# Performance work log

Hardware: AMD Instinct MI355X
Metric: run time of the kernel (lower is better)

## Reference

```python
import jax, jax.numpy as jnp
import numpy as np

N_NODES = 50000
N_EDGES = 800000
D = 128


def _graph_conv(x, W, b, src, dst, n_nodes):
    """DGL GraphConv with norm='both': D_in^{-1/2} A D_out^{-1/2} X W + b."""
    ones = jnp.ones((src.shape[0],), dtype=x.dtype)
    out_deg = jax.ops.segment_sum(ones, src, num_segments=n_nodes)
    in_deg = jax.ops.segment_sum(ones, dst, num_segments=n_nodes)
    out_norm = jax.lax.rsqrt(jnp.maximum(out_deg, 1.0))  # [N]
    in_norm = jax.lax.rsqrt(jnp.maximum(in_deg, 1.0))    # [N]
    # scale src features, transform (in_feats == out_feats so order is free), aggregate
    h = (x * out_norm[:, None]) @ W                       # [N, D]
    msgs = h[src]                                         # [E, D] gather
    agg = jax.ops.segment_sum(msgs, dst, num_segments=n_nodes)  # [N, D] scatter-add
    return agg * in_norm[:, None] + b


def setup_inputs() -> dict:
    key = jax.random.key(0)
    ks = jax.random.split(key, 8)
    x = jax.random.normal(ks[0], (N_NODES, D), dtype=jnp.float32)
    src = jax.random.randint(ks[1], (N_EDGES,), 0, N_NODES, dtype=jnp.int64)
    dst = jax.random.randint(ks[2], (N_EDGES,), 0, N_NODES, dtype=jnp.int64)
    scale = 1.0 / np.sqrt(D)
    W1 = jax.random.normal(ks[3], (D, D), dtype=jnp.float32) * scale
    W2 = jax.random.normal(ks[4], (D, D), dtype=jnp.float32) * scale
    W3 = jax.random.normal(ks[5], (D, D), dtype=jnp.float32) * scale
    b1 = jnp.zeros((D,), dtype=jnp.float32)
    b2 = jnp.zeros((D,), dtype=jnp.float32)
    b3 = jnp.zeros((D,), dtype=jnp.float32)
    return {"x": x, "src": src, "dst": dst,
            "W1": W1, "b1": b1, "W2": W2, "b2": b2, "W3": W3, "b3": b3}


def reference(x, src, dst, W1, b1, W2, b2, W3, b3):
    h = _graph_conv(x, W1, b1, src, dst, N_NODES)
    h = jax.nn.relu(h)
    h = _graph_conv(h, W2, b2, src, dst, N_NODES)
    h = jax.nn.relu(h)
    h = _graph_conv(h, W3, b3, src, dst, N_NODES)
    return h
```

## Files before the change

### kernel.cpp

```cpp
#include <hip/hip_runtime.h>
#include <hip/hip_fp16.h>

#define D 128
#define HB 128
#define HT 1024
#define WMAX 12800

struct alignas(16) H8 { __half2 h[4]; };
typedef _Float16 v8h __attribute__((ext_vector_type(8)));
typedef float v4f __attribute__((ext_vector_type(4)));

__global__ __launch_bounds__(HT) void hist_kernel(const int* __restrict__ src,
                                                  const int* __restrict__ dst,
                                                  unsigned* __restrict__ partial_out,
                                                  unsigned* __restrict__ partial_in,
                                                  unsigned char* __restrict__ lrank,
                                                  const float* __restrict__ W1,
                                                  const float* __restrict__ W2,
                                                  const float* __restrict__ W3,
                                                  _Float16* __restrict__ wt,
                                                  int nE, int W, int epb) {
    const int t = threadIdx.x;
    if ((int)blockIdx.x >= 2 * HB) {
        const int l = blockIdx.x - 2 * HB;
        const float* Wsrc = (l == 0) ? W1 : ((l == 1) ? W2 : W3);
        _Float16* o = wt + (size_t)l * D * D;
        for (int i = t; i < D * D; i += HT) {
            const int k = i >> 7, n = i & 127;
            o[n * D + k] = (_Float16)Wsrc[i];
        }
        return;
    }
    __shared__ unsigned lcnt[WMAX];
    const bool is_dst = (blockIdx.x < HB);
    const int b = is_dst ? blockIdx.x : (blockIdx.x - HB);
    for (int i = t; i < W; i += HT) lcnt[i] = 0;
    __syncthreads();
    const int e0 = b * epb;
    const int e1 = min(nE, e0 + epb);
    if (is_dst) {
        for (int e = e0 + t; e < e1; e += HT) {
            const int d = dst[e];
            const unsigned sh = (unsigned)(d & 3) * 8u;
            const unsigned old = atomicAdd(&lcnt[d >> 2], 1u << sh);
            lrank[e] = (unsigned char)((old >> sh) & 0xffu);
        }
    } else {
        for (int e = e0 + t; e < e1; e += HT) {
            const int s = src[e];
            atomicAdd(&lcnt[s >> 2], 1u << ((unsigned)(s & 3) * 8u));
        }
    }
    __syncthreads();
    unsigned* g = (is_dst ? partial_in : partial_out) + (size_t)b * W;
    for (int i = t; i < W; i += HT) g[i] = lcnt[i];
}

__global__ __launch_bounds__(256) void reduce_hist_kernel(const unsigned* __restrict__ partial_out,
                                                          const unsigned* __restrict__ partial_in,
                                                          unsigned* __restrict__ offs_in,
                                                          int* __restrict__ cnt_out,
                                                          int* __restrict__ cnt_in,
                                                          int W, int n, int nbW) {
    const bool is_dst = ((int)blockIdx.x < nbW);
    const int w = (is_dst ? blockIdx.x : (blockIdx.x - nbW)) * 256 + threadIdx.x;
    if (w >= W) return;
    unsigned run = 0;
    if (is_dst) {
#pragma unroll 16
        for (int b = 0; b < HB; ++b) {
            const unsigned c = partial_in[(size_t)b * W + w];
            offs_in[(size_t)b * W + w] = run;
            run += c;
        }
    } else {
#pragma unroll 16
        for (int b = 0; b < HB; ++b) run += partial_out[(size_t)b * W + w];
    }
    int* cnt = is_dst ? cnt_in : cnt_out;
    const int n0 = w * 4;
    const int4 c4 = make_int4((int)(run & 0xffu), (int)((run >> 8) & 0xffu),
                              (int)((run >> 16) & 0xffu), (int)((run >> 24) & 0xffu));
    if (n0 + 3 < n) {
        *(int4*)&cnt[n0] = c4;
    } else {
        const int* cp = &c4.x;
        for (int i = 0; i < 4 && n0 + i < n; ++i) cnt[n0 + i] = cp[i];
    }
}

__global__ __launch_bounds__(1024) void scan_block_kernel(const int* __restrict__ deg,
                                                          int* __restrict__ rp,
                                                          int* __restrict__ bsum, int n) {
    __shared__ int wsum[16];
    const int t = threadIdx.x;
    const int lane = t & 63;
    const int wid = t >> 6;
    const int i = blockIdx.x * 1024 + t;
    const int v = (i < n) ? deg[i] : 0;
    int s = v;
#pragma unroll
    for (int off = 1; off < 64; off <<= 1) {
        int u = __shfl_up(s, off, 64);
        if (lane >= off) s += u;
    }
    if (lane == 63) wsum[wid] = s;
    __syncthreads();
    if (wid == 0) {
        int ws = (lane < 16) ? wsum[lane] : 0;
#pragma unroll
        for (int off = 1; off < 16; off <<= 1) {
            int u = __shfl_up(ws, off, 64);
            if (lane >= off) ws += u;
        }
        if (lane < 16) wsum[lane] = ws;
    }
    __syncthreads();
    const int excl = s - v + ((wid > 0) ? wsum[wid - 1] : 0);
    if (i < n) rp[i] = excl;
    if (t == 0) bsum[blockIdx.x] = wsum[15];
}

__global__ __launch_bounds__(1024) void finalize_kernel(int* __restrict__ rp,
                                                        const int* __restrict__ bsum,
                                                        const int* __restrict__ cnt_out,
                                                        const int* __restrict__ cnt_in,
                                                        float* __restrict__ onorm,
                                                        float* __restrict__ inorm,
                                                        int n, int nb, int nE) {
    __shared__ int prefix_s;
    const int t = threadIdx.x;
    if (t < 64) {
        int v = (t < nb && t < (int)blockIdx.x) ? bsum[t] : 0;
#pragma unroll
        for (int off = 1; off < 64; off <<= 1) v += __shfl_xor(v, off, 64);
        if (t == 0) prefix_s = v;
    }
    __syncthreads();
    const int i = blockIdx.x * 1024 + t;
    if (i < n) {
        rp[i] += prefix_s;
        onorm[i] = rsqrtf(fmaxf((float)cnt_out[i], 1.0f));
        inorm[i] = rsqrtf(fmaxf((float)cnt_in[i], 1.0f));
    }
    if (blockIdx.x == 0 && t == 0) rp[n] = nE;
}

__global__ __launch_bounds__(1024) void gemm1_fill_kernel(
    const float* __restrict__ x, const _Float16* __restrict__ wt,
    const float* __restrict__ onorm, __half* __restrict__ y1, int nrows,
    const int* __restrict__ src, const int* __restrict__ dst,
    const unsigned char* __restrict__ lrank, const unsigned* __restrict__ offs_in,
    const int* __restrict__ rp, int* __restrict__ srcs_sorted,
    int nE, int epb, int W, int nGemmBlocks) {
    __shared__ _Float16 sA[128 * 136];
    __shared__ _Float16 sB[128 * 136];
    const int t = threadIdx.x;

    if ((int)blockIdx.x >= nGemmBlocks) {
        const int e = (blockIdx.x - nGemmBlocks) * 1024 + t;
        if (e < nE) {
            const int d = dst[e];
            const int b = e / epb;
            const unsigned off =
                (offs_in[(size_t)b * W + (d >> 2)] >> ((unsigned)(d & 3) * 8u)) & 0xffu;
            srcs_sorted[rp[d] + (int)off + (int)lrank[e]] = src[e];
        }
        return;
    }

    const int row0 = blockIdx.x * 128;
    const int rr = t >> 4;
    const int c8 = t & 15;
#pragma unroll
    for (int pass = 0; pass < 2; ++pass) {
        const int row = pass * 64 + rr;
        *(float4*)&sB[row * 136 + c8 * 8] = *(const float4*)&wt[(size_t)row * D + c8 * 8];
        const int grow = row0 + row;
        float4 u0 = make_float4(0.f, 0.f, 0.f, 0.f);
        float4 u1 = u0;
        if (grow < nrows) {
            const float* ap = x + (size_t)grow * D + c8 * 8;
            u0 = ((const float4*)ap)[0];
            u1 = ((const float4*)ap)[1];
        }
        v8h hv;
        hv[0] = (_Float16)u0.x; hv[1] = (_Float16)u0.y;
        hv[2] = (_Float16)u0.z; hv[3] = (_Float16)u0.w;
        hv[4] = (_Float16)u1.x; hv[5] = (_Float16)u1.y;
        hv[6] = (_Float16)u1.z; hv[7] = (_Float16)u1.w;
        *(v8h*)&sA[row * 136 + c8 * 8] = hv;
    }
    __syncthreads();

    const int w = t >> 6;
    const int lane = t & 63;
    const int m16 = lane & 15;
    const int quad = lane >> 4;
    const int rt = w >> 1;
    const int ch = w & 1;

    v4f c[4];
#pragma unroll
    for (int ct = 0; ct < 4; ++ct) c[ct] = (v4f){0.f, 0.f, 0.f, 0.f};

#pragma unroll
    for (int ks = 0; ks < 4; ++ks) {
        const v8h a = *(const v8h*)&sA[(rt * 16 + m16) * 136 + ks * 32 + quad * 8];
#pragma unroll
        for (int ct = 0; ct < 4; ++ct) {
            const v8h b = *(const v8h*)&sB[((ch * 4 + ct) * 16 + m16) * 136 + ks * 32 + quad * 8];
            c[ct] = __builtin_amdgcn_mfma_f32_16x16x32_f16(a, b, c[ct], 0, 0, 0);
        }
    }

#pragma unroll
    for (int r = 0; r < 4; ++r) {
        const int row = row0 + rt * 16 + quad * 4 + r;
        if (row < nrows) {
            const float osc = onorm[row];
#pragma unroll
            for (int ct = 0; ct < 4; ++ct) {
                const int col = (ch * 4 + ct) * 16 + m16;
                y1[(size_t)row * D + col] = __float2half(c[ct][r] * osc);
            }
        }
    }
}

template <bool EPI>
__global__ __launch_bounds__(256) void aggregate_kernel(const __half* __restrict__ xh,
                                                        const float* __restrict__ onorm,
                                                        const float* __restrict__ inorm,
                                                        const float* __restrict__ bias,
                                                        const int* __restrict__ rp,
                                                        const int* __restrict__ srcs,
                                                        __half* __restrict__ agg, int n_nodes) {
    const int node = blockIdx.x * 4 + (threadIdx.x >> 6);
    const int lane = threadIdx.x & 63;
    const int rg = lane >> 4;
    const int c8 = lane & 15;
    if (node >= n_nodes) return;
    const int e0 = rp[node];
    const int e1 = rp[node + 1];

    float acc0[8], acc1[8];
#pragma unroll
    for (int j = 0; j < 8; ++j) { acc0[j] = 0.f; acc1[j] = 0.f; }

    auto accum = [&](float* acc, const H8 v) {
#pragma unroll
        for (int j = 0; j < 4; ++j) {
            acc[2 * j]     += __low2float(v.h[j]);
            acc[2 * j + 1] += __high2float(v.h[j]);
        }
    };

    int e = e0;
    for (; e + 16 <= e1; e += 16) {
        const int s0 = srcs[e + rg];
        const int s1 = srcs[e + 4 + rg];
        const int s2 = srcs[e + 8 + rg];
        const int s3 = srcs[e + 12 + rg];
        const H8 v0 = ((const H8*)(xh + (size_t)s0 * D))[c8];
        const H8 v1 = ((const H8*)(xh + (size_t)s1 * D))[c8];
        const H8 v2 = ((const H8*)(xh + (size_t)s2 * D))[c8];
        const H8 v3 = ((const H8*)(xh + (size_t)s3 * D))[c8];
        accum(acc0, v0); accum(acc1, v1); accum(acc0, v2); accum(acc1, v3);
    }
    for (; e + 4 <= e1; e += 4) {
        const int s0 = srcs[e + rg];
        accum(acc0, ((const H8*)(xh + (size_t)s0 * D))[c8]);
    }
    if (e < e1 && rg < (e1 - e)) {
        const int s0 = srcs[e + rg];
        accum(acc1, ((const H8*)(xh + (size_t)s0 * D))[c8]);
    }

    float r[8];
#pragma unroll
    for (int j = 0; j < 8; ++j) r[j] = acc0[j] + acc1[j];
#pragma unroll
    for (int off = 16; off < 64; off <<= 1)
#pragma unroll
        for (int j = 0; j < 8; ++j) r[j] += __shfl_xor(r[j], off, 64);

    if (rg == 0) {
        if (EPI) {
            const float inm = inorm[node];
            const float onm = onorm[node];
            const float4 bv0 = ((const float4*)bias)[c8 * 2];
            const float4 bv1 = ((const float4*)bias)[c8 * 2 + 1];
            const float* bp0 = &bv0.x;
            const float* bp1 = &bv1.x;
#pragma unroll
            for (int j = 0; j < 4; ++j) {
                r[j]     = fmaxf(fmaf(r[j],     inm, bp0[j]), 0.f) * onm;
                r[j + 4] = fmaxf(fmaf(r[j + 4], inm, bp1[j]), 0.f) * onm;
            }
        }
        H8 h;
#pragma unroll
        for (int j = 0; j < 4; ++j) h.h[j] = __floats2half2_rn(r[2 * j], r[2 * j + 1]);
        ((H8*)(agg + (size_t)node * D))[c8] = h;
    }
}

template <bool FULL, bool RELU, bool OSCALE, bool OUT16>
__global__ __launch_bounds__(256) void gemm_mfma_kernel(const __half* __restrict__ Ah,
                                                        const _Float16* __restrict__ Wt,
                                                        const float* __restrict__ bias,
                                                        const float* __restrict__ inorm,
                                                        const float* __restrict__ onorm,
                                                        void* __restrict__ outv, int nrows) {
    __shared__ _Float16 sA[128 * 136];
    __shared__ _Float16 sB[128 * 136];
    const int t = threadIdx.x;
    const int row0 = blockIdx.x * 128;
    const int rr = t >> 4;
    const int c8 = t & 15;

#pragma unroll
    for (int pass = 0; pass < 8; ++pass) {
        const int row = pass * 16 + rr;
        *(float4*)&sB[row * 136 + c8 * 8] = *(const float4*)&Wt[(size_t)row * D + c8 * 8];
        const int grow = row0 + row;
        float4 v = make_float4(0.f, 0.f, 0.f, 0.f);
        if (grow < nrows)
            v = *(const float4*)((const _Float16*)Ah + (size_t)grow * D + c8 * 8);
        *(float4*)&sA[row * 136 + c8 * 8] = v;
    }
    __syncthreads();

    const int w = t >> 6;
    const int lane = t & 63;
    const int m16 = lane & 15;
    const int quad = lane >> 4;

    v4f c[2][8];
#pragma unroll
    for (int rt = 0; rt < 2; ++rt)
#pragma unroll
        for (int ct = 0; ct < 8; ++ct) c[rt][ct] = (v4f){0.f, 0.f, 0.f, 0.f};

#pragma unroll
    for (int ks = 0; ks < 4; ++ks) {
        v8h afr[2], bfr[8];
#pragma unroll
        for (int rt = 0; rt < 2; ++rt)
            afr[rt] = *(const v8h*)&sA[(w * 32 + rt * 16 + m16) * 136 + ks * 32 + quad * 8];
#pragma unroll
        for (int ct = 0; ct < 8; ++ct)
            bfr[ct] = *(const v8h*)&sB[(ct * 16 + m16) * 136 + ks * 32 + quad * 8];
#pragma unroll
        for (int rt = 0; rt < 2; ++rt)
#pragma unroll
            for (int ct = 0; ct < 8; ++ct)
                c[rt][ct] = __builtin_amdgcn_mfma_f32_16x16x32_f16(afr[rt], bfr[ct], c[rt][ct], 0, 0, 0);
    }

#pragma unroll
    for (int rt = 0; rt < 2; ++rt) {
#pragma unroll
        for (int r = 0; r < 4; ++r) {
            const int row = row0 + w * 32 + rt * 16 + quad * 4 + r;
            if (row < nrows) {
                const float inm = FULL ? inorm[row] : 1.0f;
                const float osc = OSCALE ? onorm[row] : 1.0f;
#pragma unroll
                for (int ct = 0; ct < 8; ++ct) {
                    const int col = ct * 16 + m16;
                    float v = c[rt][ct][r];
                    if (FULL) v = fmaf(v, inm, bias[col]);
                    if (RELU) v = fmaxf(v, 0.f);
                    if (OSCALE) v *= osc;
                    if (OUT16) ((__half*)outv)[(size_t)row * D + col] = __float2half(v);
                    else       ((float*)outv)[(size_t)row * D + col] = v;
                }
            }
        }
    }
}

extern "C" void kernel_launch(void* const* d_in, const int* in_sizes, int n_in,
                              void* d_out, int out_size, void* d_ws, size_t ws_size,
                              hipStream_t stream) {
    const float* x   = (const float*)d_in[0];
    const int*   src = (const int*)d_in[1];
    const int*   dst = (const int*)d_in[2];
    const float* W1  = (const float*)d_in[3];
    const float* b1  = (const float*)d_in[4];
    const float* W2  = (const float*)d_in[5];
    const float* b2  = (const float*)d_in[6];
    const float* W3  = (const float*)d_in[7];
    const float* b3  = (const float*)d_in[8];

    const int N = in_sizes[0] / D;
    const int E = in_sizes[1];

    char* p = (char*)d_ws;
    auto alloc = [&](size_t bytes) -> void* {
        void* r = (void*)p;
        p += (bytes + 255) & ~(size_t)255;
        return r;
    };
    int*           cnt_out = (int*)alloc((size_t)N * 4);
    int*           cnt_in  = (int*)alloc((size_t)N * 4);
    int*           rp      = (int*)alloc((size_t)(N + 1) * 4);
    int*           bsum    = (int*)alloc(1024 * 4);
    float*         onorm   = (float*)alloc((size_t)N * 4);
    float*         inorm   = (float*)alloc((size_t)N * 4);
    int*           srcs    = (int*)alloc((size_t)E * 4);
    unsigned char* lrank   = (unsigned char*)alloc((size_t)E);
    _Float16*      wt      = (_Float16*)alloc((size_t)3 * D * D * 2);
    __half*        hbuf0   = (__half*)alloc((size_t)N * D * 2);
    __half*        hbuf1   = (__half*)alloc((size_t)N * D * 2);
    char*          scratch = (char*)alloc((size_t)3 * HB * ((N + 3) / 4) * 4);

    const int W = (N + 3) / 4;
    const int epb = (E + HB - 1) / HB;
    unsigned* partial_in  = (unsigned*)scratch;
    unsigned* partial_out = partial_in + (size_t)HB * W;
    unsigned* offs_in     = partial_out + (size_t)HB * W;
    __half*   abuf        = (__half*)scratch;
    float*    outf        = (float*)d_out;

    const int nb = (N + 1023) / 1024;
    const int nbW = (W + 255) / 256;
    const int gemmGrid = (N + 127) / 128;
    const int fillGrid = (E + 1023) / 1024;
    const int aggGrid = (N + 3) / 4;

    hist_kernel<<<2 * HB + 3, HT, 0, stream>>>(src, dst, partial_out, partial_in, lrank,
                                               W1, W2, W3, wt, E, W, epb);
    reduce_hist_kernel<<<2 * nbW, 256, 0, stream>>>(partial_out, partial_in, offs_in,
                                                    cnt_out, cnt_in, W, N, nbW);
    scan_block_kernel<<<nb, 1024, 0, stream>>>(cnt_in, rp, bsum, N);
    finalize_kernel<<<nb, 1024, 0, stream>>>(rp, bsum, cnt_out, cnt_in, onorm, inorm, N, nb, E);

    gemm1_fill_kernel<<<gemmGrid + fillGrid, 1024, 0, stream>>>(
        x, wt, onorm, hbuf0, N,
        src, dst, lrank, offs_in, rp, srcs, E, epb, W, gemmGrid);

    aggregate_kernel<true><<<aggGrid, 256, 0, stream>>>(
        hbuf0, onorm, inorm, b1, rp, srcs, hbuf1, N);
    aggregate_kernel<false><<<aggGrid, 256, 0, stream>>>(
        hbuf1, onorm, inorm, b2, rp, srcs, abuf, N);
    gemm_mfma_kernel<true, true, true, true><<<gemmGrid, 256, 0, stream>>>(
        abuf, wt + (size_t)D * D, b2, inorm, onorm, hbuf0, N);
    aggregate_kernel<false><<<aggGrid, 256, 0, stream>>>(
        hbuf0, onorm, inorm, b3, rp, srcs, abuf, N);
    gemm_mfma_kernel<true, false, false, false><<<gemmGrid, 256, 0, stream>>>(
        abuf, wt + (size_t)2 * D * D, b3, inorm, onorm, outf, N);
}
```

Before: 245.5 us.

## Split aggregation feature columns into per-XCD slices to localize L2 working set

The aggregate kernel now assigns each block a 32-column slice of the feature row, chosen from the block index modulo 8. The intent is that each XCD only gathers a quarter of every source row, which shrinks its L2 working set and raises hit rates on the random gather. Each node is now processed by four blocks instead of one, so every block rereads the node's edge indices and row pointers. Index loads and output stores are also made nontemporal. The mapping relies on the hardware dispatching blocks round-robin across 8 XCDs.

```diff
diff --git a/kernel.cpp b/kernel.cpp
--- a/kernel.cpp
+++ b/kernel.cpp
@@ -9,6 +9,7 @@
 struct alignas(16) H8 { __half2 h[4]; };
 typedef _Float16 v8h __attribute__((ext_vector_type(8)));
 typedef float v4f __attribute__((ext_vector_type(4)));
+typedef int v4i __attribute__((ext_vector_type(4)));
 
 __global__ __launch_bounds__(HT) void hist_kernel(const int* __restrict__ src,
                                                   const int* __restrict__ dst,
@@ -235,14 +236,19 @@
                                                         const float* __restrict__ bias,
                                                         const int* __restrict__ rp,
                                                         const int* __restrict__ srcs,
-                                                        __half* __restrict__ agg, int n_nodes) {
-    const int node = blockIdx.x * 4 + (threadIdx.x >> 6);
+                                                        __half* __restrict__ agg,
+                                                        int n_nodes, int ngroups) {
+    const unsigned b = blockIdx.x;
+    const int xcd = (int)(b & 7u);
+    const int slice = xcd & 3;
+    const int node = ((xcd >> 2) * ngroups + (int)(b >> 3)) * 4 + ((int)threadIdx.x >> 6);
     const int lane = threadIdx.x & 63;
-    const int rg = lane >> 4;
-    const int c8 = lane & 15;
+    const int rg = lane >> 2;
+    const int c4 = lane & 3;
     if (node >= n_nodes) return;
     const int e0 = rp[node];
     const int e1 = rp[node + 1];
+    const __half* xbase = xh + (slice << 5);
 
     float acc0[8], acc1[8];
 #pragma unroll
@@ -257,31 +263,29 @@
     };
 
     int e = e0;
-    for (; e + 16 <= e1; e += 16) {
-        const int s0 = srcs[e + rg];
-        const int s1 = srcs[e + 4 + rg];
-        const int s2 = srcs[e + 8 + rg];
-        const int s3 = srcs[e + 12 + rg];
-        const H8 v0 = ((const H8*)(xh + (size_t)s0 * D))[c8];
-        const H8 v1 = ((const H8*)(xh + (size_t)s1 * D))[c8];
-        const H8 v2 = ((const H8*)(xh + (size_t)s2 * D))[c8];
-        const H8 v3 = ((const H8*)(xh + (size_t)s3 * D))[c8];
-        accum(acc0, v0); accum(acc1, v1); accum(acc0, v2); accum(acc1, v3);
-    }
-    for (; e + 4 <= e1; e += 4) {
-        const int s0 = srcs[e + rg];
-        accum(acc0, ((const H8*)(xh + (size_t)s0 * D))[c8]);
+    for (; e + 32 <= e1; e += 32) {
+        const int s0 = __builtin_nontemporal_load(srcs + e + rg);
+        const int s1 = __builtin_nontemporal_load(srcs + e + 16 + rg);
+        const H8 v0 = ((const H8*)(xbase + (size_t)s0 * D))[c4];
+        const H8 v1 = ((const H8*)(xbase + (size_t)s1 * D))[c4];
+        accum(acc0, v0);
+        accum(acc1, v1);
+    }
+    if (e + 16 <= e1) {
+        const int s0 = __builtin_nontemporal_load(srcs + e + rg);
+        accum(acc0, ((const H8*)(xbase + (size_t)s0 * D))[c4]);
+        e += 16;
     }
     if (e < e1 && rg < (e1 - e)) {
-        const int s0 = srcs[e + rg];
-        accum(acc1, ((const H8*)(xh + (size_t)s0 * D))[c8]);
+        const int s0 = __builtin_nontemporal_load(srcs + e + rg);
+        accum(acc1, ((const H8*)(xbase + (size_t)s0 * D))[c4]);
     }
 
     float r[8];
 #pragma unroll
     for (int j = 0; j < 8; ++j) r[j] = acc0[j] + acc1[j];
 #pragma unroll
-    for (int off = 16; off < 64; off <<= 1)
+    for (int off = 4; off < 64; off <<= 1)
 #pragma unroll
         for (int j = 0; j < 8; ++j) r[j] += __shfl_xor(r[j], off, 64);
 
@@ -289,8 +293,8 @@
         if (EPI) {
             const float inm = inorm[node];
             const float onm = onorm[node];
-            const float4 bv0 = ((const float4*)bias)[c8 * 2];
-            const float4 bv1 = ((const float4*)bias)[c8 * 2 + 1];
+            const float4 bv0 = ((const float4*)bias)[slice * 8 + c4 * 2];
+            const float4 bv1 = ((const float4*)bias)[slice * 8 + c4 * 2 + 1];
             const float* bp0 = &bv0.x;
             const float* bp1 = &bv1.x;
 #pragma unroll
@@ -302,7 +306,8 @@
         H8 h;
 #pragma unroll
         for (int j = 0; j < 4; ++j) h.h[j] = __floats2half2_rn(r[2 * j], r[2 * j + 1]);
-        ((H8*)(agg + (size_t)node * D))[c8] = h;
+        v4i* op = (v4i*)(agg + (size_t)node * D + (slice << 5)) + c4;
+        __builtin_nontemporal_store(*(const v4i*)&h, op);
     }
 }
 
@@ -429,7 +434,8 @@
     const int nbW = (W + 255) / 256;
     const int gemmGrid = (N + 127) / 128;
     const int fillGrid = (E + 1023) / 1024;
-    const int aggGrid = (N + 3) / 4;
+    const int aggGroups = (((N + 3) / 4) + 1) / 2;
+    const int aggGrid = 8 * aggGroups;
 
     hist_kernel<<<2 * HB + 3, HT, 0, stream>>>(src, dst, partial_out, partial_in, lrank,
                                                W1, W2, W3, wt, E, W, epb);
@@ -443,13 +449,13 @@
         src, dst, lrank, offs_in, rp, srcs, E, epb, W, gemmGrid);
 
     aggregate_kernel<true><<<aggGrid, 256, 0, stream>>>(
-        hbuf0, onorm, inorm, b1, rp, srcs, hbuf1, N);
+        hbuf0, onorm, inorm, b1, rp, srcs, hbuf1, N, aggGroups);
     aggregate_kernel<false><<<aggGrid, 256, 0, stream>>>(
-        hbuf1, onorm, inorm, b2, rp, srcs, abuf, N);
+        hbuf1, onorm, inorm, b2, rp, srcs, abuf, N, aggGroups);
     gemm_mfma_kernel<true, true, true, true><<<gemmGrid, 256, 0, stream>>>(
         abuf, wt + (size_t)D * D, b2, inorm, onorm, hbuf0, N);
     aggregate_kernel<false><<<aggGrid, 256, 0, stream>>>(
-        hbuf0, onorm, inorm, b3, rp, srcs, abuf, N);
+        hbuf0, onorm, inorm, b3, rp, srcs, abuf, N, aggGroups);
     gemm_mfma_kernel<true, false, false, false><<<gemmGrid, 256, 0, stream>>>(
         abuf, wt + (size_t)2 * D * D, b3, inorm, onorm, outf, N);
 }
```

Measured after the change: 392.3 us. +59.8%, slower.
